# Kernel optimization log

Hardware: AMD Instinct MI355X
Metric: run time of the kernel (lower is better)

## Reference

```python
import jax, jax.numpy as jnp
from jax import lax
import numpy as np

# ---- static APPM geometry (MMAL-Net config: input 448, stride 32 -> 14x14 fm) ----
STRIDE = 32
FM = 14
RATIOS = [[4, 4], [3, 5], [5, 3],
          [6, 6], [5, 7], [7, 5],
          [8, 8], [6, 10], [10, 6], [7, 9], [9, 7], [7, 10], [10, 7]]
N_LIST = [3, 2, 1]          # proposals per ratio-group -> proposalN = 6
IOU_THRESHS = [0.25, 0.25, 0.25]
GROUP_RATIO_SPLITS = [3, 6, 13]  # ratios 0:3, 3:6, 6:13


def _window_num(r):
    return (FM - r[0] + 1) * (FM - r[1] + 1)


def _build_coords():
    # indices2coordinates: window (i,j) of ratio (rh,rw) -> pixel box, inclusive ends
    coords = []
    for rh, rw in RATIOS:
        rows, cols = FM - rh + 1, FM - rw + 1
        ii, jj = np.meshgrid(np.arange(rows), np.arange(cols), indexing='ij')
        x0 = ii.reshape(-1) * STRIDE
        y0 = jj.reshape(-1) * STRIDE
        x1 = x0 + rh * STRIDE - 1
        y1 = y0 + rw * STRIDE - 1
        coords.append(np.stack([x0, y0, x1, y1], 1))
    return np.concatenate(coords, 0).astype(np.float32)

COORDS = jnp.asarray(_build_coords())  # [917, 4]
WINDOW_NUMS = [_window_num(r) for r in RATIOS]
_g1 = sum(WINDOW_NUMS[:3]); _g2 = sum(WINDOW_NUMS[3:6]); _g3 = sum(WINDOW_NUMS[6:])
GROUPS = [(0, _g1), (_g1, _g1 + _g2), (_g1 + _g2, _g1 + _g2 + _g3)]  # (0,361),(361,602),(602,917)


def _argmax_mask(logits):
    # mask = 0.7 everywhere, 1.0 at per-row argmax
    B, C = logits.shape
    one_hot = jax.nn.one_hot(jnp.argmax(logits, axis=1), C, dtype=logits.dtype)
    return 0.7 + 0.3 * one_hot


def _nms_group(scores, coords, n_pick, thresh):
    # greedy descending-score NMS; scores [W], coords [W,4]
    x0, y0, x1, y1 = coords[:, 0], coords[:, 1], coords[:, 2], coords[:, 3]
    areas = (x1 - x0 + 1.0) * (y1 - y0 + 1.0)

    def step(carry, _):
        valid, last = carry
        masked = jnp.where(valid, scores, -jnp.inf)
        idx = jnp.argmax(masked).astype(jnp.int32)
        idx = jnp.where(valid.any(), idx, last)  # pad by repeating last pick
        ix0, iy0, ix1, iy1 = coords[idx]
        lx = jnp.minimum(x1, ix1) - jnp.maximum(x0, ix0) + 1.0
        ly = jnp.minimum(y1, iy1) - jnp.maximum(y0, iy0) + 1.0
        inter = jnp.where((lx < 0) | (ly < 0), 0.0, lx * ly)
        iou = inter / (areas + areas[idx] - inter)
        valid = valid & (iou <= thresh)  # also suppresses idx itself (iou == 1)
        return (valid, idx), idx

    init = (jnp.ones(scores.shape[0], dtype=bool), jnp.int32(0))
    (_, _), picks = lax.scan(step, init, None, length=n_pick)
    return picks  # [n_pick] int32


def _appm(local_fm):
    # avgpool over each ratio then sum over channels == channel-sum then 2D mean pool
    B = local_fm.shape[0]
    fm_sum = jnp.sum(local_fm, axis=1)  # [B,14,14]
    per_ratio = []
    for rh, rw in RATIOS:
        pooled = lax.reduce_window(fm_sum, jnp.float32(0.0), lax.add,
                                   (1, rh, rw), (1, 1, 1), 'VALID') / (rh * rw)
        per_ratio.append(pooled.reshape(B, -1))
    all_scores = jnp.concatenate(per_ratio, axis=1)  # [B, 917]

    picks = []
    for (s, e), n_pick, thr in zip(GROUPS, N_LIST, IOU_THRESHS):
        g = jax.vmap(lambda sc: _nms_group(sc, COORDS[s:e], n_pick, thr))(all_scores[:, s:e])
        picks.append(g + s)
    proposalN_indices = jnp.concatenate(picks, axis=1)  # [B, 6]
    proposalN_windows_scores = jnp.take_along_axis(all_scores, proposalN_indices, axis=1)
    return proposalN_indices, proposalN_windows_scores, all_scores


def setup_inputs() -> dict:
    key = jax.random.key(0)
    ks = jax.random.split(key, 6)
    B, C, NC, BIT = 256, 512, 200, 48
    return {
        'local_fm': jax.random.normal(ks[0], (B, C, 14, 14), jnp.float32),
        'local_embeddings': jax.random.normal(ks[1], (B, C), jnp.float32),
        'W_cls': jax.random.normal(ks[2], (NC, C), jnp.float32) * 0.02,
        'b_cls': jax.random.normal(ks[3], (NC,), jnp.float32) * 0.02,
        'W_hash': jax.random.normal(ks[4], (BIT, NC), jnp.float32) * 0.02,
        'b_hash': jax.random.normal(ks[5], (BIT,), jnp.float32) * 0.02,
    }


def reference(local_fm, local_embeddings, W_cls, b_cls, W_hash, b_hash):
    # classification head + per-row argmax masking + hash head (Tanh)
    local_logits = local_embeddings @ W_cls.T + b_cls          # [B, num_classes]
    masked = local_logits * _argmax_mask(local_logits)
    local_hash_code = jnp.tanh(masked @ W_hash.T + b_hash)     # [B, bit]
    # APPM region proposal on detached feature map
    proposalN_indices, proposalN_windows_scores, window_scores = _appm(
        lax.stop_gradient(local_fm))
    return (local_hash_code, local_logits, proposalN_indices,
            proposalN_windows_scores, window_scores)
```

## Files before the change

kernel.cpp:

```cpp
#include <hip/hip_runtime.h>
#include <math.h>

#define NW 917

__constant__ int c_off[13]  = {0,121,241,361,442,522,602,651,696,741,789,837,877};
__constant__ int c_rh[13]   = {4,3,5,6,5,7,8,6,10,7,9,7,10};
__constant__ int c_rw[13]   = {4,5,3,6,7,5,8,10,6,9,7,10,7};
__constant__ int c_cols[13] = {11,10,12,9,8,10,7,5,9,6,8,5,8};

__device__ inline void decode_w(int w, int& r, int& i, int& j){
    int rr = 0;
    #pragma unroll
    for (int k = 1; k < 13; ++k) if (w >= c_off[k]) rr = k;
    int loc = w - c_off[rr];
    int cols = c_cols[rr];
    r = rr; i = loc / cols; j = loc - i * cols;
}

__device__ inline unsigned long long nms_key(float v, int w){
    unsigned u = __float_as_uint(v);
    u = (u & 0x80000000u) ? ~u : (u | 0x80000000u);
    return ((unsigned long long)u << 32) | (unsigned)(0xFFFFFFFFu - (unsigned)w);
}

__device__ inline unsigned long long shfl_xor_u64(unsigned long long x, int m){
    unsigned lo = (unsigned)x, hi = (unsigned)(x >> 32);
    lo = __shfl_xor(lo, m);
    hi = __shfl_xor(hi, m);
    return ((unsigned long long)hi << 32) | lo;
}

__global__ __launch_bounds__(256) void fused1_kernel(const float* __restrict__ fm,
                                                     const float* __restrict__ E,
                                                     const float* __restrict__ Wc,
                                                     const float* __restrict__ bc,
                                                     const float* __restrict__ Wh,
                                                     const float* __restrict__ bh,
                                                     float* __restrict__ partial,
                                                     float* __restrict__ out_hash,
                                                     float* __restrict__ out_logits){
    int t = threadIdx.x;
    int lane = t & 63, wv = t >> 6;
    if (blockIdx.x < 1024){
        int b = blockIdx.x >> 2, part = blockIdx.x & 3;
        __shared__ float4 red[4][49];
        const float4* base = (const float4*)(fm + (size_t)b * 512 * 196)
                             + (size_t)(part * 128) * 49;
        if (lane < 49){
            float4 acc = {0.f,0.f,0.f,0.f};
            int c0 = wv * 32;
            #pragma unroll 8
            for (int k = 0; k < 32; ++k){
                float4 v = base[(size_t)(c0 + k) * 49 + lane];
                acc.x += v.x; acc.y += v.y; acc.z += v.z; acc.w += v.w;
            }
            red[wv][lane] = acc;
        }
        __syncthreads();
        if (t < 49){
            float4 s0 = red[0][t], s1 = red[1][t], s2 = red[2][t], s3 = red[3][t];
            float4 s;
            s.x = (s0.x + s1.x) + (s2.x + s3.x);
            s.y = (s0.y + s1.y) + (s2.y + s3.y);
            s.z = (s0.z + s1.z) + (s2.z + s3.z);
            s.w = (s0.w + s1.w) + (s2.w + s3.w);
            ((float4*)partial)[(blockIdx.x) * 49 + t] = s;
        }
    } else {
        int b = blockIdx.x - 1024;
        __shared__ float emb[512];
        __shared__ float lg[200];
        __shared__ float mk[200];
        __shared__ unsigned long long wredc[4];
        emb[t]       = E[b * 512 + t];
        emb[t + 256] = E[b * 512 + 256 + t];
        __syncthreads();
        float lv = 0.f;
        if (t < 200){
            const float4* w4 = (const float4*)(Wc + (size_t)t * 512);
            float acc = bc[t];
            #pragma unroll 16
            for (int k = 0; k < 128; ++k){
                float4 w = w4[k];
                acc += emb[4*k]*w.x + emb[4*k+1]*w.y + emb[4*k+2]*w.z + emb[4*k+3]*w.w;
            }
            lg[t] = acc;
            out_logits[(size_t)b * 200 + t] = acc;
            lv = acc;
        }
        unsigned long long key = (t < 200) ? nms_key(lv, t) : 0ULL;
        #pragma unroll
        for (int off = 32; off > 0; off >>= 1){
            unsigned long long o = shfl_xor_u64(key, off);
            if (o > key) key = o;
        }
        if (lane == 0) wredc[wv] = key;
        __syncthreads();
        unsigned long long ka = wredc[0] > wredc[1] ? wredc[0] : wredc[1];
        unsigned long long kb = wredc[2] > wredc[3] ? wredc[2] : wredc[3];
        if (kb > ka) ka = kb;
        int amax = (int)(0xFFFFFFFFu - (unsigned)(ka & 0xFFFFFFFFu));
        if (t < 200) mk[t] = lg[t] * (t == amax ? 1.0f : 0.7f);
        __syncthreads();
        if (t < 48){
            const float4* w4 = (const float4*)(Wh + (size_t)t * 200);
            float acc = bh[t];
            #pragma unroll
            for (int k = 0; k < 50; ++k){
                float4 w = w4[k];
                acc += mk[4*k]*w.x + mk[4*k+1]*w.y + mk[4*k+2]*w.z + mk[4*k+3]*w.w;
            }
            out_hash[b * 48 + t] = tanhf(acc);
        }
    }
}

__global__ __launch_bounds__(256) void appm_kernel(const float* __restrict__ partial,
                                                   float* __restrict__ out_scores,
                                                   float* __restrict__ out_idx,
                                                   float* __restrict__ out_psc){
    int b = blockIdx.x, t = threadIdx.x;
    int lane = t & 63, wv = t >> 6;
    __shared__ float fm[196];
    __shared__ float R[14][15];
    __shared__ float I[15][15];
    __shared__ float s[NW];
    __shared__ unsigned long long wred[4];

    if (t < 196){
        const float* p = partial + (size_t)b * 784 + t;
        fm[t] = (p[0] + p[196]) + (p[392] + p[588]);
    }
    __syncthreads();
    if (t < 14){
        float run = 0.f;
        R[t][0] = 0.f;
        for (int j = 0; j < 14; ++j){ run += fm[t * 14 + j]; R[t][j + 1] = run; }
    }
    __syncthreads();
    if (t < 15){
        float run = 0.f;
        I[0][t] = 0.f;
        for (int i = 0; i < 14; ++i){ run += R[i][t]; I[i + 1][t] = run; }
    }
    __syncthreads();
    for (int w = t; w < NW; w += 256){
        int r, i, j; decode_w(w, r, i, j);
        int rh = c_rh[r], rw = c_rw[r];
        float sum = I[i + rh][j + rw] - I[i][j + rw] - I[i + rh][j] + I[i][j];
        float sc = sum / (float)(rh * rw);
        s[w] = sc;
        out_scores[(size_t)b * NW + w] = sc;
    }
    __syncthreads();

    const int gs_[3] = {0, 361, 602};
    const int ge_[3] = {361, 602, NW};
    const int np_[3] = {3, 2, 1};
    int slot = 0;
    for (int g = 0; g < 3; ++g){
        int gs = gs_[g], ge = ge_[g];
        int w0 = gs + t, w1 = gs + t + 256;
        bool has0 = w0 < ge, has1 = w1 < ge;
        float x00=0,y00=0,x10=0,y10=0,a0=1.f;
        float x01=0,y01=0,x11=0,y11=0,a1=1.f;
        if (has0){
            int r,i,j; decode_w(w0,r,i,j);
            x00 = i*32.f; y00 = j*32.f;
            x10 = x00 + c_rh[r]*32.f - 1.f; y10 = y00 + c_rw[r]*32.f - 1.f;
            a0  = (float)(c_rh[r]*32 * c_rw[r]*32);
        }
        if (has1){
            int r,i,j; decode_w(w1,r,i,j);
            x01 = i*32.f; y01 = j*32.f;
            x11 = x01 + c_rh[r]*32.f - 1.f; y11 = y01 + c_rw[r]*32.f - 1.f;
            a1  = (float)(c_rh[r]*32 * c_rw[r]*32);
        }
        bool v0 = true, v1 = true;
        int last = 0;
        for (int p = 0; p < np_[g]; ++p){
            unsigned long long key = 0ULL;
            if (has0 && v0) key = nms_key(s[w0], w0);
            if (has1 && v1){
                unsigned long long k2 = nms_key(s[w1], w1);
                if (k2 > key) key = k2;
            }
            #pragma unroll
            for (int off = 32; off > 0; off >>= 1){
                unsigned long long o = shfl_xor_u64(key, off);
                if (o > key) key = o;
            }
            if (lane == 0) wred[wv] = key;
            __syncthreads();
            unsigned long long ka = wred[0] > wred[1] ? wred[0] : wred[1];
            unsigned long long kb = wred[2] > wred[3] ? wred[2] : wred[3];
            if (kb > ka) ka = kb;
            int pick = (ka == 0ULL) ? last
                                    : (int)(0xFFFFFFFFu - (unsigned)(ka & 0xFFFFFFFFu));
            __syncthreads();
            last = pick;
            int pr, pi, pj; decode_w(pick, pr, pi, pj);
            float px0 = pi*32.f, py0 = pj*32.f;
            float px1 = px0 + c_rh[pr]*32.f - 1.f, py1 = py0 + c_rw[pr]*32.f - 1.f;
            float pa  = (float)(c_rh[pr]*32 * c_rw[pr]*32);
            if (has0 && v0){
                float lx = fminf(x10,px1) - fmaxf(x00,px0) + 1.f;
                float ly = fminf(y10,py1) - fmaxf(y00,py0) + 1.f;
                float inter = (lx < 0.f || ly < 0.f) ? 0.f : lx * ly;
                float iou = inter / (a0 + pa - inter);
                v0 = (iou <= 0.25f);
            }
            if (has1 && v1){
                float lx = fminf(x11,px1) - fmaxf(x01,px0) + 1.f;
                float ly = fminf(y11,py1) - fmaxf(y01,py0) + 1.f;
                float inter = (lx < 0.f || ly < 0.f) ? 0.f : lx * ly;
                float iou = inter / (a1 + pa - inter);
                v1 = (iou <= 0.25f);
            }
            if (t == 0){
                out_idx[b * 6 + slot] = (float)pick;
                out_psc[b * 6 + slot] = s[pick];
            }
            slot++;
        }
    }
}

extern "C" void kernel_launch(void* const* d_in, const int* in_sizes, int n_in,
                              void* d_out, int out_size, void* d_ws, size_t ws_size,
                              hipStream_t stream) {
    const float* fm = (const float*)d_in[0];
    const float* E  = (const float*)d_in[1];
    const float* Wc = (const float*)d_in[2];
    const float* bc = (const float*)d_in[3];
    const float* Wh = (const float*)d_in[4];
    const float* bh = (const float*)d_in[5];
    float* out        = (float*)d_out;
    float* out_hash   = out;
    float* out_logits = out + 12288;
    float* out_idx    = out + 63488;
    float* out_psc    = out + 65024;
    float* out_scores = out + 66560;
    float* partial    = (float*)d_ws;

    hipLaunchKernelGGL(fused1_kernel, dim3(1280), dim3(256), 0, stream,
                       fm, E, Wc, bc, Wh, bh, partial, out_hash, out_logits);
    hipLaunchKernelGGL(appm_kernel,   dim3(256),  dim3(256), 0, stream,
                       partial, out_scores, out_idx, out_psc);
}
```

Measured before the change: 187.3 us.

## Fuse channel reduction, heads and APPM into one 1024-thread-per-batch kernel

Merges the two kernels into one. Each block of 1024 threads handles one batch row: it reduces all 512 channels of the feature map, runs the APPM scoring and NMS, then the classification and hash heads. This removes the second launch and the partial-sum round trip through workspace memory. In exchange the grid drops from 1280 to 256 blocks, so fewer blocks are available to saturate bandwidth on the dominant 100MB feature-map read. The heads also now run serially after NMS inside the same block.

```diff
diff --git a/kernel.cpp b/kernel.cpp
--- a/kernel.cpp
+++ b/kernel.cpp
@@ -30,112 +30,58 @@
     return ((unsigned long long)hi << 32) | lo;
 }
 
-__global__ __launch_bounds__(256) void fused1_kernel(const float* __restrict__ fm,
-                                                     const float* __restrict__ E,
-                                                     const float* __restrict__ Wc,
-                                                     const float* __restrict__ bc,
-                                                     const float* __restrict__ Wh,
-                                                     const float* __restrict__ bh,
-                                                     float* __restrict__ partial,
-                                                     float* __restrict__ out_hash,
-                                                     float* __restrict__ out_logits){
-    int t = threadIdx.x;
-    int lane = t & 63, wv = t >> 6;
-    if (blockIdx.x < 1024){
-        int b = blockIdx.x >> 2, part = blockIdx.x & 3;
-        __shared__ float4 red[4][49];
-        const float4* base = (const float4*)(fm + (size_t)b * 512 * 196)
-                             + (size_t)(part * 128) * 49;
-        if (lane < 49){
-            float4 acc = {0.f,0.f,0.f,0.f};
-            int c0 = wv * 32;
-            #pragma unroll 8
-            for (int k = 0; k < 32; ++k){
-                float4 v = base[(size_t)(c0 + k) * 49 + lane];
-                acc.x += v.x; acc.y += v.y; acc.z += v.z; acc.w += v.w;
-            }
-            red[wv][lane] = acc;
-        }
-        __syncthreads();
-        if (t < 49){
-            float4 s0 = red[0][t], s1 = red[1][t], s2 = red[2][t], s3 = red[3][t];
-            float4 s;
-            s.x = (s0.x + s1.x) + (s2.x + s3.x);
-            s.y = (s0.y + s1.y) + (s2.y + s3.y);
-            s.z = (s0.z + s1.z) + (s2.z + s3.z);
-            s.w = (s0.w + s1.w) + (s2.w + s3.w);
-            ((float4*)partial)[(blockIdx.x) * 49 + t] = s;
-        }
-    } else {
-        int b = blockIdx.x - 1024;
-        __shared__ float emb[512];
-        __shared__ float lg[200];
-        __shared__ float mk[200];
-        __shared__ unsigned long long wredc[4];
-        emb[t]       = E[b * 512 + t];
-        emb[t + 256] = E[b * 512 + 256 + t];
-        __syncthreads();
-        float lv = 0.f;
-        if (t < 200){
-            const float4* w4 = (const float4*)(Wc + (size_t)t * 512);
-            float acc = bc[t];
-            #pragma unroll 16
-            for (int k = 0; k < 128; ++k){
-                float4 w = w4[k];
-                acc += emb[4*k]*w.x + emb[4*k+1]*w.y + emb[4*k+2]*w.z + emb[4*k+3]*w.w;
-            }
-            lg[t] = acc;
-            out_logits[(size_t)b * 200 + t] = acc;
-            lv = acc;
-        }
-        unsigned long long key = (t < 200) ? nms_key(lv, t) : 0ULL;
-        #pragma unroll
-        for (int off = 32; off > 0; off >>= 1){
-            unsigned long long o = shfl_xor_u64(key, off);
-            if (o > key) key = o;
-        }
-        if (lane == 0) wredc[wv] = key;
-        __syncthreads();
-        unsigned long long ka = wredc[0] > wredc[1] ? wredc[0] : wredc[1];
-        unsigned long long kb = wredc[2] > wredc[3] ? wredc[2] : wredc[3];
-        if (kb > ka) ka = kb;
-        int amax = (int)(0xFFFFFFFFu - (unsigned)(ka & 0xFFFFFFFFu));
-        if (t < 200) mk[t] = lg[t] * (t == amax ? 1.0f : 0.7f);
-        __syncthreads();
-        if (t < 48){
-            const float4* w4 = (const float4*)(Wh + (size_t)t * 200);
-            float acc = bh[t];
-            #pragma unroll
-            for (int k = 0; k < 50; ++k){
-                float4 w = w4[k];
-                acc += mk[4*k]*w.x + mk[4*k+1]*w.y + mk[4*k+2]*w.z + mk[4*k+3]*w.w;
-            }
-            out_hash[b * 48 + t] = tanhf(acc);
-        }
-    }
-}
-
-__global__ __launch_bounds__(256) void appm_kernel(const float* __restrict__ partial,
-                                                   float* __restrict__ out_scores,
-                                                   float* __restrict__ out_idx,
-                                                   float* __restrict__ out_psc){
+__global__ __launch_bounds__(1024) void mono_kernel(const float* __restrict__ fm,
+                                                    const float* __restrict__ E,
+                                                    const float* __restrict__ Wc,
+                                                    const float* __restrict__ bc,
+                                                    const float* __restrict__ Wh,
+                                                    const float* __restrict__ bh,
+                                                    float* __restrict__ out_hash,
+                                                    float* __restrict__ out_logits,
+                                                    float* __restrict__ out_idx,
+                                                    float* __restrict__ out_psc,
+                                                    float* __restrict__ out_scores){
     int b = blockIdx.x, t = threadIdx.x;
     int lane = t & 63, wv = t >> 6;
-    __shared__ float fm[196];
+
+    __shared__ float4 red[16][49];
+    __shared__ float fmS[196];
     __shared__ float R[14][15];
     __shared__ float I[15][15];
     __shared__ float s[NW];
-    __shared__ unsigned long long wred[4];
-
-    if (t < 196){
-        const float* p = partial + (size_t)b * 784 + t;
-        fm[t] = (p[0] + p[196]) + (p[392] + p[588]);
-    }
-    __syncthreads();
+    __shared__ unsigned long long wred[16];
+    __shared__ float emb[512];
+    __shared__ float lg[200];
+    __shared__ float mk[200];
+
+    const float4* base = (const float4*)(fm + (size_t)b * 512 * 196);
+    if (lane < 49){
+        float4 acc = {0.f,0.f,0.f,0.f};
+        int c0 = wv * 32;
+        #pragma unroll 8
+        for (int k = 0; k < 32; ++k){
+            float4 v = base[(size_t)(c0 + k) * 49 + lane];
+            acc.x += v.x; acc.y += v.y; acc.z += v.z; acc.w += v.w;
+        }
+        red[wv][lane] = acc;
+    }
+    if (t < 512) emb[t] = E[b * 512 + t];
+    __syncthreads();
+    if (t < 49){
+        float4 a = red[0][t];
+        #pragma unroll
+        for (int k = 1; k < 16; ++k){
+            float4 v = red[k][t];
+            a.x += v.x; a.y += v.y; a.z += v.z; a.w += v.w;
+        }
+        ((float4*)fmS)[t] = a;
+    }
+    __syncthreads();
+
     if (t < 14){
         float run = 0.f;
         R[t][0] = 0.f;
-        for (int j = 0; j < 14; ++j){ run += fm[t * 14 + j]; R[t][j + 1] = run; }
+        for (int j = 0; j < 14; ++j){ run += fmS[t * 14 + j]; R[t][j + 1] = run; }
     }
     __syncthreads();
     if (t < 15){
@@ -144,13 +90,14 @@
         for (int i = 0; i < 14; ++i){ run += R[i][t]; I[i + 1][t] = run; }
     }
     __syncthreads();
-    for (int w = t; w < NW; w += 256){
-        int r, i, j; decode_w(w, r, i, j);
+
+    if (t < NW){
+        int r, i, j; decode_w(t, r, i, j);
         int rh = c_rh[r], rw = c_rw[r];
         float sum = I[i + rh][j + rw] - I[i][j + rw] - I[i + rh][j] + I[i][j];
         float sc = sum / (float)(rh * rw);
-        s[w] = sc;
-        out_scores[(size_t)b * NW + w] = sc;
+        s[t] = sc;
+        out_scores[(size_t)b * NW + t] = sc;
     }
     __syncthreads();
 
@@ -159,32 +106,21 @@
     const int np_[3] = {3, 2, 1};
     int slot = 0;
     for (int g = 0; g < 3; ++g){
-        int gs = gs_[g], ge = ge_[g];
-        int w0 = gs + t, w1 = gs + t + 256;
-        bool has0 = w0 < ge, has1 = w1 < ge;
-        float x00=0,y00=0,x10=0,y10=0,a0=1.f;
-        float x01=0,y01=0,x11=0,y11=0,a1=1.f;
-        if (has0){
+        int gs = gs_[g], m = ge_[g] - gs;
+        bool has = t < m;
+        int w0 = gs + t;
+        float x0=0,y0=0,x1=0,y1=0,ar=1.f,sc=0.f;
+        if (has){
             int r,i,j; decode_w(w0,r,i,j);
-            x00 = i*32.f; y00 = j*32.f;
-            x10 = x00 + c_rh[r]*32.f - 1.f; y10 = y00 + c_rw[r]*32.f - 1.f;
-            a0  = (float)(c_rh[r]*32 * c_rw[r]*32);
-        }
-        if (has1){
-            int r,i,j; decode_w(w1,r,i,j);
-            x01 = i*32.f; y01 = j*32.f;
-            x11 = x01 + c_rh[r]*32.f - 1.f; y11 = y01 + c_rw[r]*32.f - 1.f;
-            a1  = (float)(c_rh[r]*32 * c_rw[r]*32);
-        }
-        bool v0 = true, v1 = true;
+            x0 = i*32.f; y0 = j*32.f;
+            x1 = x0 + c_rh[r]*32.f - 1.f; y1 = y0 + c_rw[r]*32.f - 1.f;
+            ar = (float)(c_rh[r]*32 * c_rw[r]*32);
+            sc = s[w0];
+        }
+        bool v = true;
         int last = 0;
         for (int p = 0; p < np_[g]; ++p){
-            unsigned long long key = 0ULL;
-            if (has0 && v0) key = nms_key(s[w0], w0);
-            if (has1 && v1){
-                unsigned long long k2 = nms_key(s[w1], w1);
-                if (k2 > key) key = k2;
-            }
+            unsigned long long key = (has && v) ? nms_key(sc, w0) : 0ULL;
             #pragma unroll
             for (int off = 32; off > 0; off >>= 1){
                 unsigned long long o = shfl_xor_u64(key, off);
@@ -192,37 +128,75 @@
             }
             if (lane == 0) wred[wv] = key;
             __syncthreads();
-            unsigned long long ka = wred[0] > wred[1] ? wred[0] : wred[1];
-            unsigned long long kb = wred[2] > wred[3] ? wred[2] : wred[3];
-            if (kb > ka) ka = kb;
-            int pick = (ka == 0ULL) ? last
-                                    : (int)(0xFFFFFFFFu - (unsigned)(ka & 0xFFFFFFFFu));
-            __syncthreads();
+            unsigned long long best = wred[0];
+            #pragma unroll
+            for (int k = 1; k < 16; ++k) if (wred[k] > best) best = wred[k];
+            int pick = (best == 0ULL) ? last
+                                      : (int)(0xFFFFFFFFu - (unsigned)(best & 0xFFFFFFFFu));
             last = pick;
             int pr, pi, pj; decode_w(pick, pr, pi, pj);
             float px0 = pi*32.f, py0 = pj*32.f;
             float px1 = px0 + c_rh[pr]*32.f - 1.f, py1 = py0 + c_rw[pr]*32.f - 1.f;
             float pa  = (float)(c_rh[pr]*32 * c_rw[pr]*32);
-            if (has0 && v0){
-                float lx = fminf(x10,px1) - fmaxf(x00,px0) + 1.f;
-                float ly = fminf(y10,py1) - fmaxf(y00,py0) + 1.f;
+            if (has && v){
+                float lx = fminf(x1,px1) - fmaxf(x0,px0) + 1.f;
+                float ly = fminf(y1,py1) - fmaxf(y0,py0) + 1.f;
                 float inter = (lx < 0.f || ly < 0.f) ? 0.f : lx * ly;
-                float iou = inter / (a0 + pa - inter);
-                v0 = (iou <= 0.25f);
-            }
-            if (has1 && v1){
-                float lx = fminf(x11,px1) - fmaxf(x01,px0) + 1.f;
-                float ly = fminf(y11,py1) - fmaxf(y01,py0) + 1.f;
-                float inter = (lx < 0.f || ly < 0.f) ? 0.f : lx * ly;
-                float iou = inter / (a1 + pa - inter);
-                v1 = (iou <= 0.25f);
+                float iou = inter / (ar + pa - inter);
+                v = (iou <= 0.25f);
             }
             if (t == 0){
                 out_idx[b * 6 + slot] = (float)pick;
                 out_psc[b * 6 + slot] = s[pick];
             }
             slot++;
-        }
+            __syncthreads();
+        }
+    }
+
+    float tot = 0.f;
+    if (t < 400){
+        int row = t >> 1, part = t & 1;
+        const float4* w4 = (const float4*)(Wc + (size_t)row * 512) + part * 64;
+        const float* e = emb + part * 256;
+        float acc = (part == 0) ? bc[row] : 0.f;
+        #pragma unroll 8
+        for (int k = 0; k < 64; ++k){
+            float4 w = w4[k];
+            acc += e[4*k]*w.x + e[4*k+1]*w.y + e[4*k+2]*w.z + e[4*k+3]*w.w;
+        }
+        tot = acc + __shfl_xor(acc, 1);
+        if (part == 0){
+            lg[row] = tot;
+            out_logits[(size_t)b * 200 + row] = tot;
+        }
+    }
+    unsigned long long key = (t < 400 && !(t & 1)) ? nms_key(tot, t >> 1) : 0ULL;
+    #pragma unroll
+    for (int off = 32; off > 0; off >>= 1){
+        unsigned long long o = shfl_xor_u64(key, off);
+        if (o > key) key = o;
+    }
+    if (lane == 0) wred[wv] = key;
+    __syncthreads();
+    unsigned long long best = wred[0];
+    #pragma unroll
+    for (int k = 1; k < 16; ++k) if (wred[k] > best) best = wred[k];
+    int amax = (int)(0xFFFFFFFFu - (unsigned)(best & 0xFFFFFFFFu));
+    if (t < 200) mk[t] = lg[t] * (t == amax ? 1.0f : 0.7f);
+    __syncthreads();
+    if (t < 96){
+        int row = t >> 1, part = t & 1;
+        const float4* w4 = (const float4*)(Wh + (size_t)row * 200) + part * 25;
+        const float* mm = mk + part * 100;
+        float acc = (part == 0) ? bh[row] : 0.f;
+        #pragma unroll
+        for (int k = 0; k < 25; ++k){
+            float4 w = w4[k];
+            acc += mm[4*k]*w.x + mm[4*k+1]*w.y + mm[4*k+2]*w.z + mm[4*k+3]*w.w;
+        }
+        float tt = acc + __shfl_xor(acc, 1);
+        if (part == 0) out_hash[b * 48 + row] = tanhf(tt);
     }
 }
 
@@ -241,10 +215,8 @@
     float* out_idx    = out + 63488;
     float* out_psc    = out + 65024;
     float* out_scores = out + 66560;
-    float* partial    = (float*)d_ws;
-
-    hipLaunchKernelGGL(fused1_kernel, dim3(1280), dim3(256), 0, stream,
-                       fm, E, Wc, bc, Wh, bh, partial, out_hash, out_logits);
-    hipLaunchKernelGGL(appm_kernel,   dim3(256),  dim3(256), 0, stream,
-                       partial, out_scores, out_idx, out_psc);
-}
+
+    hipLaunchKernelGGL(mono_kernel, dim3(256), dim3(1024), 0, stream,
+                       fm, E, Wc, bc, Wh, bh,
+                       out_hash, out_logits, out_idx, out_psc, out_scores);
+}
```

Result: faster. 180.0 us (-3.9%).
